# Kernel optimization log

Hardware: AMD Instinct MI355X
Metric: run time of the kernel (lower is better)

Reference implementation:

```python
import jax, jax.numpy as jnp
import numpy as np

D_MODEL = 1024
D_FF = 4096
NUM_EXPERTS = 8
TOP_K = 2


def setup_inputs() -> dict:
    key = jax.random.key(0)
    ks = jax.random.split(key, 9)
    s = 0.02
    x = jax.random.normal(ks[0], (2, 2048, D_MODEL), dtype=jnp.float32)
    Wg = jax.random.normal(ks[1], (D_MODEL, NUM_EXPERTS), dtype=jnp.float32) * s
    bg = jnp.zeros((NUM_EXPERTS,), dtype=jnp.float32)
    W1 = jax.random.normal(ks[2], (NUM_EXPERTS, D_MODEL, D_FF), dtype=jnp.float32) * s
    b1 = jnp.zeros((NUM_EXPERTS, D_FF), dtype=jnp.float32)
    W3 = jax.random.normal(ks[3], (NUM_EXPERTS, D_MODEL, D_FF), dtype=jnp.float32) * s
    b3 = jnp.zeros((NUM_EXPERTS, D_FF), dtype=jnp.float32)
    W2 = jax.random.normal(ks[4], (NUM_EXPERTS, D_FF, D_MODEL), dtype=jnp.float32) * s
    b2 = jnp.zeros((NUM_EXPERTS, D_MODEL), dtype=jnp.float32)
    return {"x": x, "Wg": Wg, "bg": bg, "W1": W1, "b1": b1,
            "W3": W3, "b3": b3, "W2": W2, "b2": b2}


def reference(x, Wg, bg, W1, b1, W3, b3, W2, b2):
    # Gate (eval mode: no gaussian noise, no dropout)
    logits = x @ Wg + bg                                  # [b, s, E]
    probs = jax.nn.softmax(logits, axis=-1)
    top_v, top_i = jax.lax.top_k(probs, TOP_K)            # [b, s, K]
    top_v = top_v / (top_v.sum(axis=-1, keepdims=True) + 1e-6)
    # combine[b,s,e] = sum_k top_v[b,s,k] * 1[top_i[b,s,k]==e]
    onehot = jax.nn.one_hot(top_i, NUM_EXPERTS, dtype=x.dtype)  # [b, s, K, E]
    combine = jnp.einsum('bsk,bske->bse', top_v, onehot)        # [b, s, E]

    out = jnp.zeros_like(x)
    for e in range(NUM_EXPERTS):
        # SwiGLU expert FFN applied densely; masked-out tokens zeroed by combine weight
        h = jax.nn.silu(x @ W1[e] + b1[e]) * (x @ W3[e] + b3[e])   # [b, s, d_ff]
        out = out + combine[..., e:e + 1] * (h @ W2[e] + b2[e])
    return out
```

## Files before the change

### kernel.cpp

```cpp
#include <hip/hip_runtime.h>
#include <stdint.h>

#define D_MODEL 1024
#define D_FF    4096
#define NE      8
#define T_TOK   4096
#define R_TOT   8192

typedef float f32x4 __attribute__((ext_vector_type(4)));
typedef __bf16 bf16x8 __attribute__((ext_vector_type(8)));
typedef unsigned short ushort_t;

__device__ __forceinline__ ushort_t f2bf(float f) {
    unsigned int u = __float_as_uint(f);
    u += 0x7FFFu + ((u >> 16) & 1u);
    return (ushort_t)(u >> 16);
}

__device__ __forceinline__ void async16(const void* g, const void* l) {
    __builtin_amdgcn_global_load_lds(
        (const __attribute__((address_space(1))) unsigned int*)(uintptr_t)g,
        (__attribute__((address_space(3))) unsigned int*)(uintptr_t)l,
        16, 0, 0);
}

__global__ __launch_bounds__(256) void k_gate(
    const float* __restrict__ x, const float* __restrict__ Wg, const float* __restrict__ bg,
    int* __restrict__ topi, float* __restrict__ topw, int* __restrict__ counts)
{
    int wave = threadIdx.x >> 6, lane = threadIdx.x & 63;
    int t = blockIdx.x * 4 + wave;
    const float* xr = x + (size_t)t * D_MODEL;
    float acc[NE];
#pragma unroll
    for (int e = 0; e < NE; ++e) acc[e] = 0.f;
#pragma unroll
    for (int i = 0; i < D_MODEL / 64; ++i) {
        int k = i * 64 + lane;
        float xv = xr[k];
        const float4* wgp = (const float4*)(Wg + (size_t)k * NE);
        float4 w0 = wgp[0], w1 = wgp[1];
        acc[0] += xv * w0.x; acc[1] += xv * w0.y; acc[2] += xv * w0.z; acc[3] += xv * w0.w;
        acc[4] += xv * w1.x; acc[5] += xv * w1.y; acc[6] += xv * w1.z; acc[7] += xv * w1.w;
    }
#pragma unroll
    for (int off = 32; off >= 1; off >>= 1)
#pragma unroll
        for (int e = 0; e < NE; ++e) acc[e] += __shfl_down(acc[e], off, 64);
    if (lane == 0) {
        float l[NE], m = -1e30f;
#pragma unroll
        for (int e = 0; e < NE; ++e) { l[e] = acc[e] + bg[e]; m = fmaxf(m, l[e]); }
        float p[NE], Z = 0.f;
#pragma unroll
        for (int e = 0; e < NE; ++e) { p[e] = __expf(l[e] - m); Z += p[e]; }
        float invZ = 1.f / Z;
        int i0 = 0; float v0 = -1.f;
#pragma unroll
        for (int e = 0; e < NE; ++e) { p[e] *= invZ; if (p[e] > v0) { v0 = p[e]; i0 = e; } }
        int i1 = 0; float v1 = -1.f;
#pragma unroll
        for (int e = 0; e < NE; ++e) { if (e != i0 && p[e] > v1) { v1 = p[e]; i1 = e; } }
        float denom = 1.f / (v0 + v1 + 1e-6f);
        topi[t * 2 + 0] = i0; topi[t * 2 + 1] = i1;
        topw[t * 2 + 0] = v0 * denom; topw[t * 2 + 1] = v1 * denom;
        atomicAdd(&counts[i0], 1); atomicAdd(&counts[i1], 1);
    }
}

__global__ void k_scan(const int* __restrict__ counts, int* __restrict__ offsets,
                       int* __restrict__ cursors)
{
    if (threadIdx.x == 0) {
        int acc = 0;
        for (int e = 0; e < NE; ++e) { offsets[e] = acc; cursors[e] = acc; acc += counts[e]; }
    }
}

__global__ __launch_bounds__(256) void k_scatter(
    const int* __restrict__ topi, const float* __restrict__ topw,
    int* __restrict__ cursors, int* __restrict__ btok, float* __restrict__ bw)
{
    int t = blockIdx.x * 256 + threadIdx.x;
#pragma unroll
    for (int k = 0; k < 2; ++k) {
        int e = topi[t * 2 + k];
        int p = atomicAdd(&cursors[e], 1);
        btok[p] = t;
        bw[p] = topw[t * 2 + k];
    }
}

__global__ __launch_bounds__(256) void k_gather(
    const float* __restrict__ x, const int* __restrict__ btok, ushort_t* __restrict__ Xg)
{
    int i = blockIdx.x;
    int t = btok[i];
    float4 v = ((const float4*)(x + (size_t)t * D_MODEL))[threadIdx.x];
    ushort4 o;
    o.x = f2bf(v.x); o.y = f2bf(v.y); o.z = f2bf(v.z); o.w = f2bf(v.w);
    ((ushort4*)(Xg + (size_t)i * D_MODEL))[threadIdx.x] = o;
}

__global__ __launch_bounds__(256) void k_transpose(
    const float* __restrict__ W, ushort_t* __restrict__ Wt, int K, int N)
{
    __shared__ ushort_t tile[64 * 72];
    int e = blockIdx.z;
    const float* We = W + (size_t)e * K * N;
    ushort_t* Wte = Wt + (size_t)e * K * N;
    int nb = blockIdx.x * 64, kb = blockIdx.y * 64;
    int tn4 = (threadIdx.x & 15) * 4;
    int tk = threadIdx.x >> 4;
#pragma unroll
    for (int r = 0; r < 4; ++r) {
        int k = r * 16 + tk;
        float4 v = *(const float4*)(We + (size_t)(kb + k) * N + nb + tn4);
        tile[(tn4 + 0) * 72 + k] = f2bf(v.x);
        tile[(tn4 + 1) * 72 + k] = f2bf(v.y);
        tile[(tn4 + 2) * 72 + k] = f2bf(v.z);
        tile[(tn4 + 3) * 72 + k] = f2bf(v.w);
    }
    __syncthreads();
#pragma unroll
    for (int c = 0; c < 4; ++c) {
        int chunk = c * 256 + threadIdx.x;
        int n = chunk >> 4, kc = (chunk & 15) * 4;
        ushort4 o = *(const ushort4*)&tile[n * 72 + kc];
        *(ushort4*)(Wte + (size_t)(nb + n) * K + kb + kc) = o;
    }
}

__global__ __launch_bounds__(256) void k_gemm1(
    const ushort_t* __restrict__ Xg, const ushort_t* __restrict__ W1t,
    const ushort_t* __restrict__ W3t,
    const float* __restrict__ b1, const float* __restrict__ b3,
    const int* __restrict__ counts, const int* __restrict__ offsets,
    ushort_t* __restrict__ H)
{
    __shared__ __align__(16) ushort_t sA[128 * 32];
    __shared__ __align__(16) ushort_t sB1[128 * 32];
    __shared__ __align__(16) ushort_t sB3[128 * 32];

    int tm = blockIdx.x, e = 0, cnt = 0;
    for (; e < NE; ++e) {
        cnt = counts[e];
        int nt = (cnt + 127) >> 7;
        if (tm < nt) break;
        tm -= nt;
    }
    if (e >= NE) return;
    int row0 = offsets[e] + tm * 128;
    int rows_left = cnt - tm * 128;

    int tile_n = blockIdx.y * 128;
    int tid = threadIdx.x, wave = tid >> 6, lane = tid & 63;
    int wm = (wave >> 1) * 64, wn = (wave & 1) * 64;
    int col = lane & 15, quad = lane >> 4;

    const ushort_t* W1e = W1t + (size_t)e * D_FF * D_MODEL;
    const ushort_t* W3e = W3t + (size_t)e * D_FF * D_MODEL;

    f32x4 acc1[4][4], acc3[4][4];
#pragma unroll
    for (int i = 0; i < 4; ++i)
#pragma unroll
        for (int j = 0; j < 4; ++j) {
            acc1[i][j] = (f32x4){0.f, 0.f, 0.f, 0.f};
            acc3[i][j] = (f32x4){0.f, 0.f, 0.f, 0.f};
        }

    int q0 = wave * 128 + lane;
    int q1 = wave * 128 + 64 + lane;
    int am0 = q0 >> 2, ac0 = (q0 & 3) * 8;
    int am1 = q1 >> 2, ac1 = (q1 & 3) * 8;
    unsigned ab0 = (unsigned)(wave * 2 + 0) * 512;
    unsigned ab1 = (unsigned)(wave * 2 + 1) * 512;

    for (int k0 = 0; k0 < D_MODEL; k0 += 32) {
        async16(Xg + (size_t)(row0 + am0) * D_MODEL + k0 + ac0, sA + ab0);
        async16(Xg + (size_t)(row0 + am1) * D_MODEL + k0 + ac1, sA + ab1);
        async16(W1e + (size_t)(tile_n + am0) * D_MODEL + k0 + ac0, sB1 + ab0);
        async16(W1e + (size_t)(tile_n + am1) * D_MODEL + k0 + ac1, sB1 + ab1);
        async16(W3e + (size_t)(tile_n + am0) * D_MODEL + k0 + ac0, sB3 + ab0);
        async16(W3e + (size_t)(tile_n + am1) * D_MODEL + k0 + ac1, sB3 + ab1);
        __syncthreads();
        bf16x8 a[4], u1[4], u3[4];
#pragma unroll
        for (int i = 0; i < 4; ++i) {
            a[i]  = *(const bf16x8*)(sA  + (wm + i * 16 + col) * 32 + quad * 8);
            u1[i] = *(const bf16x8*)(sB1 + (wn + i * 16 + col) * 32 + quad * 8);
            u3[i] = *(const bf16x8*)(sB3 + (wn + i * 16 + col) * 32 + quad * 8);
        }
#pragma unroll
        for (int i = 0; i < 4; ++i)
#pragma unroll
            for (int j = 0; j < 4; ++j) {
                acc1[i][j] = __builtin_amdgcn_mfma_f32_16x16x32_bf16(a[i], u1[j], acc1[i][j], 0, 0, 0);
                acc3[i][j] = __builtin_amdgcn_mfma_f32_16x16x32_bf16(a[i], u3[j], acc3[i][j], 0, 0, 0);
            }
        __syncthreads();
    }

#pragma unroll
    for (int j = 0; j < 4; ++j) {
        int n = tile_n + wn + j * 16 + col;
        float bias1 = b1[e * D_FF + n];
        float bias3 = b3[e * D_FF + n];
#pragma unroll
        for (int i = 0; i < 4; ++i) {
            int rbase = wm + i * 16 + quad * 4;
#pragma unroll
            for (int r = 0; r < 4; ++r) {
                int row = rbase + r;
                if (row < rows_left) {
                    float h1 = acc1[i][j][r] + bias1;
                    float h3 = acc3[i][j][r] + bias3;
                    float s = h1 / (1.f + __expf(-h1));
                    H[(size_t)(row0 + row) * D_FF + n] = f2bf(s * h3);
                }
            }
        }
    }
}

__global__ __launch_bounds__(256) void k_gemm2(
    const ushort_t* __restrict__ H, const ushort_t* __restrict__ W2t,
    const float* __restrict__ b2,
    const int* __restrict__ counts, const int* __restrict__ offsets,
    const int* __restrict__ btok, const float* __restrict__ bw,
    float* __restrict__ out)
{
    __shared__ __align__(16) ushort_t sA[128 * 32];
    __shared__ __align__(16) ushort_t sB[128 * 32];

    int tm = blockIdx.x, e = 0, cnt = 0;
    for (; e < NE; ++e) {
        cnt = counts[e];
        int nt = (cnt + 127) >> 7;
        if (tm < nt) break;
        tm -= nt;
    }
    if (e >= NE) return;
    int row0 = offsets[e] + tm * 128;
    int rows_left = cnt - tm * 128;

    int tile_n = blockIdx.y * 128;
    int tid = threadIdx.x, wave = tid >> 6, lane = tid & 63;
    int wm = (wave >> 1) * 64, wn = (wave & 1) * 64;
    int col = lane & 15, quad = lane >> 4;

    const ushort_t* W2e = W2t + (size_t)e * D_MODEL * D_FF;

    f32x4 acc[4][4];
#pragma unroll
    for (int i = 0; i < 4; ++i)
#pragma unroll
        for (int j = 0; j < 4; ++j) acc[i][j] = (f32x4){0.f, 0.f, 0.f, 0.f};

    int q0 = wave * 128 + lane;
    int q1 = wave * 128 + 64 + lane;
    int am0 = q0 >> 2, ac0 = (q0 & 3) * 8;
    int am1 = q1 >> 2, ac1 = (q1 & 3) * 8;
    unsigned ab0 = (unsigned)(wave * 2 + 0) * 512;
    unsigned ab1 = (unsigned)(wave * 2 + 1) * 512;

    for (int k0 = 0; k0 < D_FF; k0 += 32) {
        async16(H + (size_t)(row0 + am0) * D_FF + k0 + ac0, sA + ab0);
        async16(H + (size_t)(row0 + am1) * D_FF + k0 + ac1, sA + ab1);
        async16(W2e + (size_t)(tile_n + am0) * D_FF + k0 + ac0, sB + ab0);
        async16(W2e + (size_t)(tile_n + am1) * D_FF + k0 + ac1, sB + ab1);
        __syncthreads();
        bf16x8 a[4], b[4];
#pragma unroll
        for (int i = 0; i < 4; ++i) {
            a[i] = *(const bf16x8*)(sA + (wm + i * 16 + col) * 32 + quad * 8);
            b[i] = *(const bf16x8*)(sB + (wn + i * 16 + col) * 32 + quad * 8);
        }
#pragma unroll
        for (int i = 0; i < 4; ++i)
#pragma unroll
            for (int j = 0; j < 4; ++j)
                acc[i][j] = __builtin_amdgcn_mfma_f32_16x16x32_bf16(a[i], b[j], acc[i][j], 0, 0, 0);
        __syncthreads();
    }

    float bias[4];
#pragma unroll
    for (int j = 0; j < 4; ++j) bias[j] = b2[e * D_MODEL + tile_n + wn + j * 16 + col];

#pragma unroll
    for (int i = 0; i < 4; ++i) {
        int rbase = wm + i * 16 + quad * 4;
#pragma unroll
        for (int r = 0; r < 4; ++r) {
            int row = rbase + r;
            if (row < rows_left) {
                int g_r = row0 + row;
                int t = btok[g_r];
                float w = bw[g_r];
                float* orow = out + (size_t)t * D_MODEL + tile_n + wn + col;
#pragma unroll
                for (int j = 0; j < 4; ++j)
                    atomicAdd(orow + j * 16, w * (acc[i][j][r] + bias[j]));
            }
        }
    }
}

extern "C" void kernel_launch(void* const* d_in, const int* in_sizes, int n_in,
                              void* d_out, int out_size, void* d_ws, size_t ws_size,
                              hipStream_t stream)
{
    const float* x  = (const float*)d_in[0];
    const float* Wg = (const float*)d_in[1];
    const float* bg = (const float*)d_in[2];
    const float* W1 = (const float*)d_in[3];
    const float* b1 = (const float*)d_in[4];
    const float* W3 = (const float*)d_in[5];
    const float* b3 = (const float*)d_in[6];
    const float* W2 = (const float*)d_in[7];
    const float* b2 = (const float*)d_in[8];
    float* out = (float*)d_out;

    char* ws = (char*)d_ws;
    int*   counts  = (int*)(ws + 0);
    int*   cursors = (int*)(ws + 32);
    int*   offsets = (int*)(ws + 64);
    int*   topi    = (int*)(ws + 256);
    float* topw    = (float*)(ws + 256 + 32768);
    int*   btok    = (int*)(ws + 256 + 65536);
    float* bw      = (float*)(ws + 256 + 98304);
    char* p = ws + 131328;
    ushort_t* Xg  = (ushort_t*)p;  p += (size_t)R_TOT * D_MODEL * 2;
    ushort_t* Hb  = (ushort_t*)p;  p += (size_t)R_TOT * D_FF * 2;
    ushort_t* W1t = (ushort_t*)p;  p += (size_t)NE * D_FF * D_MODEL * 2;
    ushort_t* W3t = (ushort_t*)p;  p += (size_t)NE * D_FF * D_MODEL * 2;
    ushort_t* W2t = (ushort_t*)p;

    hipMemsetAsync(ws, 0, 64, stream);
    hipMemsetAsync(d_out, 0, (size_t)out_size * 4, stream);

    k_gate<<<dim3(T_TOK / 4), dim3(256), 0, stream>>>(x, Wg, bg, topi, topw, counts);
    k_scan<<<dim3(1), dim3(64), 0, stream>>>(counts, offsets, cursors);
    k_scatter<<<dim3(T_TOK / 256), dim3(256), 0, stream>>>(topi, topw, cursors, btok, bw);
    k_gather<<<dim3(R_TOT), dim3(256), 0, stream>>>(x, btok, Xg);
    k_transpose<<<dim3(D_FF / 64, D_MODEL / 64, NE), dim3(256), 0, stream>>>(W1, W1t, D_MODEL, D_FF);
    k_transpose<<<dim3(D_FF / 64, D_MODEL / 64, NE), dim3(256), 0, stream>>>(W3, W3t, D_MODEL, D_FF);
    k_transpose<<<dim3(D_MODEL / 64, D_FF / 64, NE), dim3(256), 0, stream>>>(W2, W2t, D_FF, D_MODEL);
    k_gemm1<<<dim3(72, D_FF / 128), dim3(256), 0, stream>>>(Xg, W1t, W3t, b1, b3, counts, offsets, Hb);
    k_gemm2<<<dim3(72, D_MODEL / 128), dim3(256), 0, stream>>>(Hb, W2t, b2, counts, offsets, btok, bw, out);
}
```

Before: 1.108 ms.

## Deepen K tile to 64 with XOR-swizzled LDS layout in expert GEMMs

Both expert GEMM kernels now stage 64-wide K slices per barrier pair instead of 32, which halves the number of __syncthreads per K loop. The LDS tile layout is XOR-swizzled on 16-byte column groups so that MFMA fragment reads avoid bank conflicts. Global load addresses are precomputed once outside the loop. Launch bounds now request two blocks per CU, and the larger shared footprint (48KB in gemm1) may limit occupancy.

```diff
diff --git a/kernel.cpp b/kernel.cpp
--- a/kernel.cpp
+++ b/kernel.cpp
@@ -131,16 +131,17 @@
     }
 }
 
-__global__ __launch_bounds__(256) void k_gemm1(
+
+__global__ __launch_bounds__(256, 2) void k_gemm1(
     const ushort_t* __restrict__ Xg, const ushort_t* __restrict__ W1t,
     const ushort_t* __restrict__ W3t,
     const float* __restrict__ b1, const float* __restrict__ b3,
     const int* __restrict__ counts, const int* __restrict__ offsets,
     ushort_t* __restrict__ H)
 {
-    __shared__ __align__(16) ushort_t sA[128 * 32];
-    __shared__ __align__(16) ushort_t sB1[128 * 32];
-    __shared__ __align__(16) ushort_t sB3[128 * 32];
+    __shared__ __align__(16) ushort_t sA[128 * 64];
+    __shared__ __align__(16) ushort_t sB1[128 * 64];
+    __shared__ __align__(16) ushort_t sB3[128 * 64];
 
     int tm = blockIdx.x, e = 0, cnt = 0;
     for (; e < NE; ++e) {
@@ -161,6 +162,26 @@
     const ushort_t* W1e = W1t + (size_t)e * D_FF * D_MODEL;
     const ushort_t* W3e = W3t + (size_t)e * D_FF * D_MODEL;
 
+    const ushort_t* gA[4]; const ushort_t* gB1[4]; const ushort_t* gB3[4];
+    unsigned ldsOff[4];
+#pragma unroll
+    for (int s = 0; s < 4; ++s) {
+        int q = (wave * 4 + s) * 64 + lane;
+        int r = q >> 3;
+        int cg = ((q & 7) ^ (r & 7)) * 8;
+        gA[s]  = Xg  + (size_t)(row0 + r) * D_MODEL + cg;
+        gB1[s] = W1e + (size_t)(tile_n + r) * D_MODEL + cg;
+        gB3[s] = W3e + (size_t)(tile_n + r) * D_MODEL + cg;
+        ldsOff[s] = (unsigned)(wave * 4 + s) * 512;
+    }
+    int swz = (quad ^ (col & 7)) * 8;
+    unsigned fA[4], fB[4];
+#pragma unroll
+    for (int i = 0; i < 4; ++i) {
+        fA[i] = (unsigned)(wm + i * 16 + col) * 64 + swz;
+        fB[i] = (unsigned)(wn + i * 16 + col) * 64 + swz;
+    }
+
     f32x4 acc1[4][4], acc3[4][4];
 #pragma unroll
     for (int i = 0; i < 4; ++i)
@@ -170,35 +191,33 @@
             acc3[i][j] = (f32x4){0.f, 0.f, 0.f, 0.f};
         }
 
-    int q0 = wave * 128 + lane;
-    int q1 = wave * 128 + 64 + lane;
-    int am0 = q0 >> 2, ac0 = (q0 & 3) * 8;
-    int am1 = q1 >> 2, ac1 = (q1 & 3) * 8;
-    unsigned ab0 = (unsigned)(wave * 2 + 0) * 512;
-    unsigned ab1 = (unsigned)(wave * 2 + 1) * 512;
-
-    for (int k0 = 0; k0 < D_MODEL; k0 += 32) {
-        async16(Xg + (size_t)(row0 + am0) * D_MODEL + k0 + ac0, sA + ab0);
-        async16(Xg + (size_t)(row0 + am1) * D_MODEL + k0 + ac1, sA + ab1);
-        async16(W1e + (size_t)(tile_n + am0) * D_MODEL + k0 + ac0, sB1 + ab0);
-        async16(W1e + (size_t)(tile_n + am1) * D_MODEL + k0 + ac1, sB1 + ab1);
-        async16(W3e + (size_t)(tile_n + am0) * D_MODEL + k0 + ac0, sB3 + ab0);
-        async16(W3e + (size_t)(tile_n + am1) * D_MODEL + k0 + ac1, sB3 + ab1);
+    for (int k0 = 0; k0 < D_MODEL; k0 += 64) {
+#pragma unroll
+        for (int s = 0; s < 4; ++s) {
+            async16(gA[s]  + k0, sA  + ldsOff[s]);
+            async16(gB1[s] + k0, sB1 + ldsOff[s]);
+            async16(gB3[s] + k0, sB3 + ldsOff[s]);
+        }
         __syncthreads();
-        bf16x8 a[4], u1[4], u3[4];
-#pragma unroll
-        for (int i = 0; i < 4; ++i) {
-            a[i]  = *(const bf16x8*)(sA  + (wm + i * 16 + col) * 32 + quad * 8);
-            u1[i] = *(const bf16x8*)(sB1 + (wn + i * 16 + col) * 32 + quad * 8);
-            u3[i] = *(const bf16x8*)(sB3 + (wn + i * 16 + col) * 32 + quad * 8);
-        }
-#pragma unroll
-        for (int i = 0; i < 4; ++i)
+#pragma unroll
+        for (int kk = 0; kk < 2; ++kk) {
+            unsigned kx = kk * 32;
+            bf16x8 u1[4], u3[4];
 #pragma unroll
             for (int j = 0; j < 4; ++j) {
-                acc1[i][j] = __builtin_amdgcn_mfma_f32_16x16x32_bf16(a[i], u1[j], acc1[i][j], 0, 0, 0);
-                acc3[i][j] = __builtin_amdgcn_mfma_f32_16x16x32_bf16(a[i], u3[j], acc3[i][j], 0, 0, 0);
-            }
+                u1[j] = *(const bf16x8*)(sB1 + (fB[j] ^ kx));
+                u3[j] = *(const bf16x8*)(sB3 + (fB[j] ^ kx));
+            }
+#pragma unroll
+            for (int i = 0; i < 4; ++i) {
+                bf16x8 a = *(const bf16x8*)(sA + (fA[i] ^ kx));
+#pragma unroll
+                for (int j = 0; j < 4; ++j) {
+                    acc1[i][j] = __builtin_amdgcn_mfma_f32_16x16x32_bf16(a, u1[j], acc1[i][j], 0, 0, 0);
+                    acc3[i][j] = __builtin_amdgcn_mfma_f32_16x16x32_bf16(a, u3[j], acc3[i][j], 0, 0, 0);
+                }
+            }
+        }
         __syncthreads();
     }
 
@@ -224,15 +243,15 @@
     }
 }
 
-__global__ __launch_bounds__(256) void k_gemm2(
+__global__ __launch_bounds__(256, 2) void k_gemm2(
     const ushort_t* __restrict__ H, const ushort_t* __restrict__ W2t,
     const float* __restrict__ b2,
     const int* __restrict__ counts, const int* __restrict__ offsets,
     const int* __restrict__ btok, const float* __restrict__ bw,
     float* __restrict__ out)
 {
-    __shared__ __align__(16) ushort_t sA[128 * 32];
-    __shared__ __align__(16) ushort_t sB[128 * 32];
+    __shared__ __align__(16) ushort_t sA[128 * 64];
+    __shared__ __align__(16) ushort_t sB[128 * 64];
 
     int tm = blockIdx.x, e = 0, cnt = 0;
     for (; e < NE; ++e) {
@@ -252,36 +271,52 @@
 
     const ushort_t* W2e = W2t + (size_t)e * D_MODEL * D_FF;
 
+    const ushort_t* gA[4]; const ushort_t* gB[4];
+    unsigned ldsOff[4];
+#pragma unroll
+    for (int s = 0; s < 4; ++s) {
+        int q = (wave * 4 + s) * 64 + lane;
+        int r = q >> 3;
+        int cg = ((q & 7) ^ (r & 7)) * 8;
+        gA[s] = H   + (size_t)(row0 + r) * D_FF + cg;
+        gB[s] = W2e + (size_t)(tile_n + r) * D_FF + cg;
+        ldsOff[s] = (unsigned)(wave * 4 + s) * 512;
+    }
+    int swz = (quad ^ (col & 7)) * 8;
+    unsigned fA[4], fB[4];
+#pragma unroll
+    for (int i = 0; i < 4; ++i) {
+        fA[i] = (unsigned)(wm + i * 16 + col) * 64 + swz;
+        fB[i] = (unsigned)(wn + i * 16 + col) * 64 + swz;
+    }
+
     f32x4 acc[4][4];
 #pragma unroll
     for (int i = 0; i < 4; ++i)
 #pragma unroll
         for (int j = 0; j < 4; ++j) acc[i][j] = (f32x4){0.f, 0.f, 0.f, 0.f};
 
-    int q0 = wave * 128 + lane;
-    int q1 = wave * 128 + 64 + lane;
-    int am0 = q0 >> 2, ac0 = (q0 & 3) * 8;
-    int am1 = q1 >> 2, ac1 = (q1 & 3) * 8;
-    unsigned ab0 = (unsigned)(wave * 2 + 0) * 512;
-    unsigned ab1 = (unsigned)(wave * 2 + 1) * 512;
-
-    for (int k0 = 0; k0 < D_FF; k0 += 32) {
-        async16(H + (size_t)(row0 + am0) * D_FF + k0 + ac0, sA + ab0);
-        async16(H + (size_t)(row0 + am1) * D_FF + k0 + ac1, sA + ab1);
-        async16(W2e + (size_t)(tile_n + am0) * D_FF + k0 + ac0, sB + ab0);
-        async16(W2e + (size_t)(tile_n + am1) * D_FF + k0 + ac1, sB + ab1);
+    for (int k0 = 0; k0 < D_FF; k0 += 64) {
+#pragma unroll
+        for (int s = 0; s < 4; ++s) {
+            async16(gA[s] + k0, sA + ldsOff[s]);
+            async16(gB[s] + k0, sB + ldsOff[s]);
+        }
         __syncthreads();
-        bf16x8 a[4], b[4];
-#pragma unroll
-        for (int i = 0; i < 4; ++i) {
-            a[i] = *(const bf16x8*)(sA + (wm + i * 16 + col) * 32 + quad * 8);
-            b[i] = *(const bf16x8*)(sB + (wn + i * 16 + col) * 32 + quad * 8);
-        }
-#pragma unroll
-        for (int i = 0; i < 4; ++i)
-#pragma unroll
-            for (int j = 0; j < 4; ++j)
-                acc[i][j] = __builtin_amdgcn_mfma_f32_16x16x32_bf16(a[i], b[j], acc[i][j], 0, 0, 0);
+#pragma unroll
+        for (int kk = 0; kk < 2; ++kk) {
+            unsigned kx = kk * 32;
+            bf16x8 b[4];
+#pragma unroll
+            for (int j = 0; j < 4; ++j) b[j] = *(const bf16x8*)(sB + (fB[j] ^ kx));
+#pragma unroll
+            for (int i = 0; i < 4; ++i) {
+                bf16x8 a = *(const bf16x8*)(sA + (fA[i] ^ kx));
+#pragma unroll
+                for (int j = 0; j < 4; ++j)
+                    acc[i][j] = __builtin_amdgcn_mfma_f32_16x16x32_bf16(a, b[j], acc[i][j], 0, 0, 0);
+            }
+        }
         __syncthreads();
     }
 
```

After: 914.9 us. 17.4% less time.

## Double-buffer LDS, swizzle layout, and split-K gemm2 across two z-slices

Applied to the files above, without the earlier changes.

Both expert GEMMs now double-buffer their LDS tiles, prefetching the next K-slice with async global-to-LDS loads while computing on the current one. The per-iteration barrier count drops from two to one. LDS rows are XOR-swizzled to reduce bank conflicts on the fragment reads. gemm2 is split along K into two z-slices that combine through the existing atomic adds, which gives more blocks for occupancy, and launch bounds hint 2–3 blocks per CU. The costs are doubled LDS use, twice the atomic traffic in gemm2, and a single barrier that relies on the async writes having completed.

```diff
diff --git a/kernel.cpp b/kernel.cpp
--- a/kernel.cpp
+++ b/kernel.cpp
@@ -131,16 +131,17 @@
     }
 }
 
-__global__ __launch_bounds__(256) void k_gemm1(
+
+__global__ __launch_bounds__(256, 2) void k_gemm1(
     const ushort_t* __restrict__ Xg, const ushort_t* __restrict__ W1t,
     const ushort_t* __restrict__ W3t,
     const float* __restrict__ b1, const float* __restrict__ b3,
     const int* __restrict__ counts, const int* __restrict__ offsets,
     ushort_t* __restrict__ H)
 {
-    __shared__ __align__(16) ushort_t sA[128 * 32];
-    __shared__ __align__(16) ushort_t sB1[128 * 32];
-    __shared__ __align__(16) ushort_t sB3[128 * 32];
+    __shared__ __align__(16) ushort_t sA[2][4096];
+    __shared__ __align__(16) ushort_t sB1[2][4096];
+    __shared__ __align__(16) ushort_t sB3[2][4096];
 
     int tm = blockIdx.x, e = 0, cnt = 0;
     for (; e < NE; ++e) {
@@ -161,6 +162,24 @@
     const ushort_t* W1e = W1t + (size_t)e * D_FF * D_MODEL;
     const ushort_t* W3e = W3t + (size_t)e * D_FF * D_MODEL;
 
+    int lr = lane >> 2, slot = lane & 3;
+    int r_s = wave * 32 + lr;
+    int cchunk = slot ^ ((r_s >> 1) & 3);
+    const ushort_t* pA  = Xg  + (size_t)(row0 + r_s) * D_MODEL + cchunk * 8;
+    const ushort_t* pB1 = W1e + (size_t)(tile_n + r_s) * D_MODEL + cchunk * 8;
+    const ushort_t* pB3 = W3e + (size_t)(tile_n + r_s) * D_MODEL + cchunk * 8;
+    const unsigned ldsb = (unsigned)wave * 1024;
+    const size_t rstep = (size_t)16 * D_MODEL;
+
+    unsigned offA[4], offB[4];
+#pragma unroll
+    for (int i = 0; i < 4; ++i) {
+        int ra = wm + i * 16 + col;
+        int rb = wn + i * 16 + col;
+        offA[i] = (unsigned)ra * 32 + (unsigned)((quad ^ ((ra >> 1) & 3)) * 8);
+        offB[i] = (unsigned)rb * 32 + (unsigned)((quad ^ ((rb >> 1) & 3)) * 8);
+    }
+
     f32x4 acc1[4][4], acc3[4][4];
 #pragma unroll
     for (int i = 0; i < 4; ++i)
@@ -170,36 +189,36 @@
             acc3[i][j] = (f32x4){0.f, 0.f, 0.f, 0.f};
         }
 
-    int q0 = wave * 128 + lane;
-    int q1 = wave * 128 + 64 + lane;
-    int am0 = q0 >> 2, ac0 = (q0 & 3) * 8;
-    int am1 = q1 >> 2, ac1 = (q1 & 3) * 8;
-    unsigned ab0 = (unsigned)(wave * 2 + 0) * 512;
-    unsigned ab1 = (unsigned)(wave * 2 + 1) * 512;
-
-    for (int k0 = 0; k0 < D_MODEL; k0 += 32) {
-        async16(Xg + (size_t)(row0 + am0) * D_MODEL + k0 + ac0, sA + ab0);
-        async16(Xg + (size_t)(row0 + am1) * D_MODEL + k0 + ac1, sA + ab1);
-        async16(W1e + (size_t)(tile_n + am0) * D_MODEL + k0 + ac0, sB1 + ab0);
-        async16(W1e + (size_t)(tile_n + am1) * D_MODEL + k0 + ac1, sB1 + ab1);
-        async16(W3e + (size_t)(tile_n + am0) * D_MODEL + k0 + ac0, sB3 + ab0);
-        async16(W3e + (size_t)(tile_n + am1) * D_MODEL + k0 + ac1, sB3 + ab1);
+    async16(pA, sA[0] + ldsb);             async16(pA + rstep, sA[0] + ldsb + 512);
+    async16(pB1, sB1[0] + ldsb);           async16(pB1 + rstep, sB1[0] + ldsb + 512);
+    async16(pB3, sB3[0] + ldsb);           async16(pB3 + rstep, sB3[0] + ldsb + 512);
+
+    int p = 0;
+    for (int it = 0; it < D_MODEL / 32; ++it) {
         __syncthreads();
-        bf16x8 a[4], u1[4], u3[4];
+        if (it + 1 < D_MODEL / 32) {
+            int ko = (it + 1) * 32;
+            int q = p ^ 1;
+            async16(pA + ko, sA[q] + ldsb);           async16(pA + ko + rstep, sA[q] + ldsb + 512);
+            async16(pB1 + ko, sB1[q] + ldsb);         async16(pB1 + ko + rstep, sB1[q] + ldsb + 512);
+            async16(pB3 + ko, sB3[q] + ldsb);         async16(pB3 + ko + rstep, sB3[q] + ldsb + 512);
+        }
+        bf16x8 u1[4], u3[4];
+#pragma unroll
+        for (int j = 0; j < 4; ++j) {
+            u1[j] = *(const bf16x8*)(sB1[p] + offB[j]);
+            u3[j] = *(const bf16x8*)(sB3[p] + offB[j]);
+        }
 #pragma unroll
         for (int i = 0; i < 4; ++i) {
-            a[i]  = *(const bf16x8*)(sA  + (wm + i * 16 + col) * 32 + quad * 8);
-            u1[i] = *(const bf16x8*)(sB1 + (wn + i * 16 + col) * 32 + quad * 8);
-            u3[i] = *(const bf16x8*)(sB3 + (wn + i * 16 + col) * 32 + quad * 8);
-        }
-#pragma unroll
-        for (int i = 0; i < 4; ++i)
+            bf16x8 a = *(const bf16x8*)(sA[p] + offA[i]);
 #pragma unroll
             for (int j = 0; j < 4; ++j) {
-                acc1[i][j] = __builtin_amdgcn_mfma_f32_16x16x32_bf16(a[i], u1[j], acc1[i][j], 0, 0, 0);
-                acc3[i][j] = __builtin_amdgcn_mfma_f32_16x16x32_bf16(a[i], u3[j], acc3[i][j], 0, 0, 0);
+                acc1[i][j] = __builtin_amdgcn_mfma_f32_16x16x32_bf16(a, u1[j], acc1[i][j], 0, 0, 0);
+                acc3[i][j] = __builtin_amdgcn_mfma_f32_16x16x32_bf16(a, u3[j], acc3[i][j], 0, 0, 0);
             }
-        __syncthreads();
+        }
+        p ^= 1;
     }
 
 #pragma unroll
@@ -224,15 +243,15 @@
     }
 }
 
-__global__ __launch_bounds__(256) void k_gemm2(
+__global__ __launch_bounds__(256, 3) void k_gemm2(
     const ushort_t* __restrict__ H, const ushort_t* __restrict__ W2t,
     const float* __restrict__ b2,
     const int* __restrict__ counts, const int* __restrict__ offsets,
     const int* __restrict__ btok, const float* __restrict__ bw,
     float* __restrict__ out)
 {
-    __shared__ __align__(16) ushort_t sA[128 * 32];
-    __shared__ __align__(16) ushort_t sB[128 * 32];
+    __shared__ __align__(16) ushort_t sA[2][4096];
+    __shared__ __align__(16) ushort_t sB[2][4096];
 
     int tm = blockIdx.x, e = 0, cnt = 0;
     for (; e < NE; ++e) {
@@ -246,48 +265,68 @@
     int rows_left = cnt - tm * 128;
 
     int tile_n = blockIdx.y * 128;
+    int zc = blockIdx.z;
+    int kz = zc * (D_FF / 2);
+
     int tid = threadIdx.x, wave = tid >> 6, lane = tid & 63;
     int wm = (wave >> 1) * 64, wn = (wave & 1) * 64;
     int col = lane & 15, quad = lane >> 4;
 
     const ushort_t* W2e = W2t + (size_t)e * D_MODEL * D_FF;
 
+    int lr = lane >> 2, slot = lane & 3;
+    int r_s = wave * 32 + lr;
+    int cchunk = slot ^ ((r_s >> 1) & 3);
+    const ushort_t* pA = H   + (size_t)(row0 + r_s) * D_FF + kz + cchunk * 8;
+    const ushort_t* pB = W2e + (size_t)(tile_n + r_s) * D_FF + kz + cchunk * 8;
+    const unsigned ldsb = (unsigned)wave * 1024;
+    const size_t rstep = (size_t)16 * D_FF;
+
+    unsigned offA[4], offB[4];
+#pragma unroll
+    for (int i = 0; i < 4; ++i) {
+        int ra = wm + i * 16 + col;
+        int rb = wn + i * 16 + col;
+        offA[i] = (unsigned)ra * 32 + (unsigned)((quad ^ ((ra >> 1) & 3)) * 8);
+        offB[i] = (unsigned)rb * 32 + (unsigned)((quad ^ ((rb >> 1) & 3)) * 8);
+    }
+
     f32x4 acc[4][4];
 #pragma unroll
     for (int i = 0; i < 4; ++i)
 #pragma unroll
         for (int j = 0; j < 4; ++j) acc[i][j] = (f32x4){0.f, 0.f, 0.f, 0.f};
 
-    int q0 = wave * 128 + lane;
-    int q1 = wave * 128 + 64 + lane;
-    int am0 = q0 >> 2, ac0 = (q0 & 3) * 8;
-    int am1 = q1 >> 2, ac1 = (q1 & 3) * 8;
-    unsigned ab0 = (unsigned)(wave * 2 + 0) * 512;
-    unsigned ab1 = (unsigned)(wave * 2 + 1) * 512;
-
-    for (int k0 = 0; k0 < D_FF; k0 += 32) {
-        async16(H + (size_t)(row0 + am0) * D_FF + k0 + ac0, sA + ab0);
-        async16(H + (size_t)(row0 + am1) * D_FF + k0 + ac1, sA + ab1);
-        async16(W2e + (size_t)(tile_n + am0) * D_FF + k0 + ac0, sB + ab0);
-        async16(W2e + (size_t)(tile_n + am1) * D_FF + k0 + ac1, sB + ab1);
+    async16(pA, sA[0] + ldsb);   async16(pA + rstep, sA[0] + ldsb + 512);
+    async16(pB, sB[0] + ldsb);   async16(pB + rstep, sB[0] + ldsb + 512);
+
+    int p = 0;
+    const int NIT = (D_FF / 2) / 32;
+    for (int it = 0; it < NIT; ++it) {
         __syncthreads();
-        bf16x8 a[4], b[4];
+        if (it + 1 < NIT) {
+            int ko = (it + 1) * 32;
+            int q = p ^ 1;
+            async16(pA + ko, sA[q] + ldsb);   async16(pA + ko + rstep, sA[q] + ldsb + 512);
+            async16(pB + ko, sB[q] + ldsb);   async16(pB + ko + rstep, sB[q] + ldsb + 512);
+        }
+        bf16x8 b[4];
+#pragma unroll
+        for (int j = 0; j < 4; ++j) b[j] = *(const bf16x8*)(sB[p] + offB[j]);
 #pragma unroll
         for (int i = 0; i < 4; ++i) {
-            a[i] = *(const bf16x8*)(sA + (wm + i * 16 + col) * 32 + quad * 8);
-            b[i] = *(const bf16x8*)(sB + (wn + i * 16 + col) * 32 + quad * 8);
-        }
-#pragma unroll
-        for (int i = 0; i < 4; ++i)
+            bf16x8 a = *(const bf16x8*)(sA[p] + offA[i]);
 #pragma unroll
             for (int j = 0; j < 4; ++j)
-                acc[i][j] = __builtin_amdgcn_mfma_f32_16x16x32_bf16(a[i], b[j], acc[i][j], 0, 0, 0);
-        __syncthreads();
+                acc[i][j] = __builtin_amdgcn_mfma_f32_16x16x32_bf16(a, b[j], acc[i][j], 0, 0, 0);
+        }
+        p ^= 1;
     }
 
     float bias[4];
 #pragma unroll
-    for (int j = 0; j < 4; ++j) bias[j] = b2[e * D_MODEL + tile_n + wn + j * 16 + col];
+    for (int j = 0; j < 4; ++j)
+        bias[j] = (zc == 0) ? b2[e * D_MODEL + tile_n + wn + j * 16 + col] : 0.f;
 
 #pragma unroll
     for (int i = 0; i < 4; ++i) {
@@ -349,5 +388,5 @@
     k_transpose<<<dim3(D_FF / 64, D_MODEL / 64, NE), dim3(256), 0, stream>>>(W3, W3t, D_MODEL, D_FF);
     k_transpose<<<dim3(D_MODEL / 64, D_FF / 64, NE), dim3(256), 0, stream>>>(W2, W2t, D_FF, D_MODEL);
     k_gemm1<<<dim3(72, D_FF / 128), dim3(256), 0, stream>>>(Xg, W1t, W3t, b1, b3, counts, offsets, Hb);
-    k_gemm2<<<dim3(72, D_MODEL / 128), dim3(256), 0, stream>>>(Hb, W2t, b2, counts, offsets, btok, bw, out);
-}
+    k_gemm2<<<dim3(72, D_MODEL / 128, 2), dim3(256), 0, stream>>>(Hb, W2t, b2, counts, offsets, btok, bw, out);
+}
```

New measurement: 998.8 us. 9.9% less time.
